# Kernel tuning notes

Measured on AMD Instinct MI355X. Metric: run time of the kernel, lower is better.

## Reference

```python
import jax, jax.numpy as jnp
import numpy as np

N_EMBD = 1024
N_HEAD = 16
B, T = 8, 1024

def setup_inputs() -> dict:
    key = jax.random.key(0)
    ks = jax.random.split(key, 5)
    s = 0.02
    return {
        'x': jax.random.normal(ks[0], (B, T, N_EMBD), dtype=jnp.float32),
        'w_attn': jax.random.normal(ks[1], (N_EMBD, 3 * N_EMBD), dtype=jnp.float32) * s,
        'b_attn': jax.random.normal(ks[2], (3 * N_EMBD,), dtype=jnp.float32) * s,
        'w_proj': jax.random.normal(ks[3], (N_EMBD, N_EMBD), dtype=jnp.float32) * s,
        'b_proj': jax.random.normal(ks[4], (N_EMBD,), dtype=jnp.float32) * s,
    }

def reference(x, w_attn, b_attn, w_proj, b_proj):
    Bb, Tt, C = x.shape
    hd = C // N_HEAD  # head dim
    qkv = x @ w_attn + b_attn                      # [B,T,3C]
    q, k, v = jnp.split(qkv, 3, axis=2)
    # [B,T,C] -> [B,H,T,hd]
    def to_heads(t):
        return t.reshape(Bb, Tt, N_HEAD, hd).transpose(0, 2, 1, 3)
    q, k, v = to_heads(q), to_heads(k), to_heads(v)
    scale = 1.0 / jnp.sqrt(jnp.asarray(hd, dtype=x.dtype))
    att = jnp.einsum('bhqd,bhkd->bhqk', q, k) * scale  # [B,H,T,T]
    causal = jnp.tril(jnp.ones((Tt, Tt), dtype=bool))  # [T,T]
    att = jnp.where(causal[None, None, :, :], att, -jnp.inf)
    att = jax.nn.softmax(att, axis=-1)
    y = jnp.einsum('bhqk,bhkd->bhqd', att, v)          # [B,H,T,hd]
    y = y.transpose(0, 2, 1, 3).reshape(Bb, Tt, C)
    y = y @ w_proj + b_proj
    return y
```

## Files before the change

kernel.cpp:

```cpp
#include <hip/hip_runtime.h>
#include <stdint.h>

#define N_EMBD 1024
#define NHEAD  16
#define HDIM   64
#define BATCH  8
#define SEQ    1024
#define MROWS  (BATCH*SEQ)

typedef __bf16 bf16x8 __attribute__((ext_vector_type(8)));
typedef float  f32x4  __attribute__((ext_vector_type(4)));

__device__ inline unsigned short f2bf(float f) {
  uint32_t u = __float_as_uint(f);
  u += 0x7FFFu + ((u >> 16) & 1u);
  return (unsigned short)(u >> 16);
}

__device__ inline f32x4 mfma_bf16(bf16x8 a, bf16x8 b, f32x4 c) {
  return __builtin_amdgcn_mfma_f32_16x16x32_bf16(a, b, c, 0, 0, 0);
}

__device__ inline void gload_lds16(const unsigned short* g, unsigned short* l) {
  __builtin_amdgcn_global_load_lds(
      (const __attribute__((address_space(1))) void*)g,
      (__attribute__((address_space(3))) void*)l,
      16, 0, 0);
}

#define DSB __builtin_amdgcn_sched_barrier(0)
#define BARRIER __builtin_amdgcn_s_barrier()
#define VMC(n) asm volatile("s_waitcnt vmcnt(" #n ")" ::: "memory")
#define LGKM0 asm volatile("s_waitcnt lgkmcnt(0)" ::: "memory"); DSB

__global__ __launch_bounds__(256) void cast_f32_bf16(
    const float* __restrict__ in, unsigned short* __restrict__ out, int n) {
  int i = (blockIdx.x * 256 + threadIdx.x) * 4;
  if (i >= n) return;
  float4 v = *(const float4*)(in + i);
  ushort4 o;
  o.x = f2bf(v.x); o.y = f2bf(v.y); o.z = f2bf(v.z); o.w = f2bf(v.w);
  *(ushort4*)(out + i) = o;
}

__global__ __launch_bounds__(256) void transpose_cast2(
    const float* __restrict__ wa, unsigned short* __restrict__ oa,
    const float* __restrict__ wp, unsigned short* __restrict__ op) {
  __shared__ unsigned short tile[64 * 72];
  const int K = 1024;
  int bx = blockIdx.x;
  const float* in; unsigned short* out; int N;
  if (bx < 48) { in = wa; out = oa; N = 3072; }
  else         { in = wp; out = op; N = 1024; bx -= 48; }
  int k0 = blockIdx.y * 64, n0 = bx * 64;
  int t = threadIdx.x;
  {
    int col = (t & 15) * 4;
#pragma unroll
    for (int it = 0; it < 4; ++it) {
      int row = (t >> 4) + it * 16;
      float4 v = *(const float4*)(in + (size_t)(k0 + row) * N + n0 + col);
      ushort4 o;
      o.x = f2bf(v.x); o.y = f2bf(v.y); o.z = f2bf(v.z); o.w = f2bf(v.w);
      *(ushort4*)&tile[row * 72 + col] = o;
    }
  }
  __syncthreads();
  {
    int kcol = (t & 7) * 8;
#pragma unroll
    for (int it = 0; it < 2; ++it) {
      int nrow = (t >> 3) + it * 32;
      alignas(16) unsigned short tmp[8];
#pragma unroll
      for (int j = 0; j < 8; ++j) tmp[j] = tile[(kcol + j) * 72 + nrow];
      *(uint4*)(out + (size_t)(n0 + nrow) * K + k0 + kcol) = *(const uint4*)tmp;
    }
  }
}

#define GEMM98_BODY(A_, Bt_)                                                    \
  __shared__ unsigned short Asl[2][8192];                                       \
  __shared__ unsigned short Bsl[2][8192];                                       \
  const int tid = threadIdx.x;                                                  \
  const int l = tid & 63, w = tid >> 6;                                         \
  const int wr = w >> 1, wc = w & 1;                                            \
  const int g = l >> 4, fr = l & 15;                                            \
  f32x4 acc[4][4];                                                              \
  _Pragma("unroll") for (int i = 0; i < 4; ++i)                                 \
    _Pragma("unroll") for (int j = 0; j < 4; ++j)                               \
      _Pragma("unroll") for (int r = 0; r < 4; ++r) acc[i][j][r] = 0.0f;        \
  const int rr = tid >> 3;                                                      \
  const int cs = ((tid & 7) * 16) ^ ((rr & 7) << 4);                            \
  const char* srcA[4]; const char* srcB[4];                                     \
  _Pragma("unroll") for (int c = 0; c < 4; ++c) {                               \
    srcA[c] = (const char*)(A_) + (size_t)(m0 + c * 32 + rr) * 2048 + cs;       \
    srcB[c] = (const char*)(Bt_) + (size_t)(n0 + c * 32 + rr) * 2048 + cs;      \
  }                                                                             \
  const int ldso = tid * 8;                                         \
  const int arow = (wr * 64 + fr) * 128;                                        \
  const int brow = (wc * 64 + fr) * 128;                                        \
  int colk[2];                                                                  \
  colk[0] = (g * 16) ^ ((fr & 7) << 4);                                         \
  colk[1] = (64 + g * 16) ^ ((fr & 7) << 4);                                    \
  _Pragma("unroll") for (int c = 0; c < 4; ++c)                                 \
    gload_lds16((const unsigned short*)(srcA[c]), &Asl[0][ldso + c * 2048]);    \
  _Pragma("unroll") for (int c = 0; c < 4; ++c)                                 \
    gload_lds16((const unsigned short*)(srcB[c]), &Bsl[0][ldso + c * 2048]);    \
  _Pragma("unroll") for (int c = 0; c < 4; ++c)                                 \
    gload_lds16((const unsigned short*)(srcA[c] + 128), &Asl[1][ldso + c * 2048]);\
  _Pragma("unroll") for (int c = 0; c < 4; ++c)                                 \
    gload_lds16((const unsigned short*)(srcB[c] + 128), &Bsl[1][ldso + c * 2048]);\
  for (int kt = 0; kt < 16; ++kt) {                                             \
    const int cur = kt & 1;                                                     \
    if (kt < 15) { VMC(8); } else { VMC(0); }                                   \
    DSB; BARRIER; DSB;                                                          \
    _Pragma("unroll") for (int ks = 0; ks < 2; ++ks) {                          \
      bf16x8 av[4], bv[4];                                                      \
      _Pragma("unroll") for (int m = 0; m < 4; ++m)                             \
        av[m] = *(const bf16x8*)((const char*)&Asl[cur][0] + arow +             \
                                 m * 16 * 128 + colk[ks]);                      \
      _Pragma("unroll") for (int n = 0; n < 4; ++n)                             \
        bv[n] = *(const bf16x8*)((const char*)&Bsl[cur][0] + brow +             \
                                 n * 16 * 128 + colk[ks]);                      \
      _Pragma("unroll") for (int n = 0; n < 4; ++n)                             \
        _Pragma("unroll") for (int m = 0; m < 4; ++m)                           \
          acc[m][n] = mfma_bf16(av[m], bv[n], acc[m][n]);                       \
    }                                                                           \
    LGKM0; BARRIER; DSB;                                                        \
    if (kt < 14) {                                                              \
      const int ko = (kt + 2) * 128;                                            \
      _Pragma("unroll") for (int c = 0; c < 4; ++c)                             \
        gload_lds16((const unsigned short*)(srcA[c] + ko),                      \
                    &Asl[cur][ldso + c * 2048]);                                \
      _Pragma("unroll") for (int c = 0; c < 4; ++c)                             \
        gload_lds16((const unsigned short*)(srcB[c] + ko),                      \
                    &Bsl[cur][ldso + c * 2048]);                                \
    }                                                                           \
  }

__global__ __launch_bounds__(256) void gemm_qkv(
    const unsigned short* __restrict__ A, const unsigned short* __restrict__ Bt,
    const float* __restrict__ bias,
    unsigned short* __restrict__ Qo, unsigned short* __restrict__ Ko,
    unsigned short* __restrict__ VTo) {
  const int bid = blockIdx.x;
  const int xcd = bid & 7;
  const int local = bid >> 3;
  const int nchunk = local >> 6;
  const int rem = local & 63;
  const int m0 = (xcd * 8 + (rem >> 3)) * 128;
  const int n0 = (nchunk * 8 + (rem & 7)) * 128;
  GEMM98_BODY(A, Bt)
#pragma unroll
  for (int i = 0; i < 4; ++i) {
    int mb = m0 + wr * 64 + i * 16 + 4 * g;
    int bidx = mb >> 10;
    int t = mb & 1023;
#pragma unroll
    for (int j = 0; j < 4; ++j) {
      int n = n0 + wc * 64 + j * 16 + fr;
      float bv2 = bias[n];
      int part = n >> 10;
      int nn2 = n & 1023;
      int h = nn2 >> 6, d = nn2 & 63;
      if (part == 2) {
        alignas(8) unsigned short pk[4];
#pragma unroll
        for (int r = 0; r < 4; ++r) pk[r] = f2bf(acc[i][j][r] + bv2);
        *(ushort4*)&VTo[((size_t)(bidx * NHEAD + h) * HDIM + d) * SEQ + t] =
            *(const ushort4*)pk;
      } else {
        unsigned short* dst = (part == 0) ? Qo : Ko;
        float scl = (part == 0) ? 0.125f : 1.0f;
        size_t base = ((size_t)(bidx * NHEAD + h) * SEQ + t) * HDIM + d;
#pragma unroll
        for (int r = 0; r < 4; ++r)
          dst[base + (size_t)r * HDIM] = f2bf((acc[i][j][r] + bv2) * scl);
      }
    }
  }
}

__global__ __launch_bounds__(256) void gemm_proj(
    const unsigned short* __restrict__ A, const unsigned short* __restrict__ Bt,
    const float* __restrict__ bias, float* __restrict__ Out) {
  const int bid = blockIdx.x;
  const int xcd = bid & 7;
  const int local = bid >> 3;
  const int m0 = (xcd * 8 + (local >> 3)) * 128;
  const int n0 = (local & 7) * 128;
  GEMM98_BODY(A, Bt)
#pragma unroll
  for (int i = 0; i < 4; ++i) {
    int mb = m0 + wr * 64 + i * 16 + 4 * g;
#pragma unroll
    for (int j = 0; j < 4; ++j) {
      int n = n0 + wc * 64 + j * 16 + fr;
      float bv2 = bias[n];
#pragma unroll
      for (int r = 0; r < 4; ++r)
        Out[(size_t)(mb + r) * N_EMBD + n] = acc[i][j][r] + bv2;
    }
  }
}

__global__ __launch_bounds__(256) void attn_kernel(
    const unsigned short* __restrict__ Q, const unsigned short* __restrict__ Kv,
    const unsigned short* __restrict__ VT, unsigned short* __restrict__ Y) {
  __shared__ unsigned short Kt[2][4096];
  __shared__ unsigned short Vt[2][4096];
  __shared__ unsigned short p_lds[4 * 32 * 72];
  __shared__ float smx[4][32];
  int tid = threadIdx.x, l = tid & 63, w = tid >> 6;
  int bid = blockIdx.x;
  int swz = (bid & 7) * 64 + (bid >> 3);
  int bh = swz >> 2;
  int pairIdx = swz & 3;
  int b = bh >> 4, h = bh & 15;
  const unsigned short* Qb = Q + (size_t)bh * SEQ * HDIM;
  const char* Kc = (const char*)(Kv + (size_t)bh * SEQ * HDIM);
  const char* Vc = (const char*)(VT + (size_t)bh * HDIM * SEQ);
  unsigned short* pw = &p_lds[w * 32 * 72];
  const int g = l >> 4;
  const int fr = l & 15;

  const int P0 = tid * 16, P1 = tid * 16 + 4096;
  const int r0 = P0 >> 7, r1 = P1 >> 7;
  const int s0 = (P0 & 127) ^ ((r0 & 7) << 4);
  const int s1 = (P1 & 127) ^ ((r1 & 7) << 4);
  const char* Kg0 = Kc + r0 * 128 + s0;
  const char* Kg1 = Kc + r1 * 128 + s1;
  const char* Vg0 = Vc + (size_t)r0 * 2048 + s0;
  const char* Vg1 = Vc + (size_t)r1 * 2048 + s1;

  const int bc = (16 * g) ^ ((l & 7) << 4);

  for (int part = 0; part < 2; ++part) {
    const int qt = (part == 0) ? pairIdx : 7 - pairIdx;
    const int q0 = qt * 128;
    const int wq = q0 + w * 32;

    bf16x8 aq[2][2];
#pragma unroll
    for (int i = 0; i < 2; ++i)
#pragma unroll
      for (int ik = 0; ik < 2; ++ik)
        aq[i][ik] = *(const bf16x8*)&Qb[(size_t)(wq + i * 16 + fr) * HDIM + ik * 32 + 8 * g];

    float mrun[2], lpart[2];
    mrun[0] = mrun[1] = 0.0f;
    lpart[0] = lpart[1] = 0.0f;
    f32x4 acc_o[2][4];
#pragma unroll
    for (int i = 0; i < 2; ++i)
#pragma unroll
      for (int jd = 0; jd < 4; ++jd)
#pragma unroll
        for (int r = 0; r < 4; ++r) acc_o[i][jd][r] = 0.0f;

    const int n_it = (q0 + 128) >> 6;

    gload_lds16((const unsigned short*)(Kg0), &Kt[0][P0 >> 1]);
    gload_lds16((const unsigned short*)(Kg1), &Kt[0][P1 >> 1]);
    gload_lds16((const unsigned short*)(Vg0), &Vt[0][P0 >> 1]);
    gload_lds16((const unsigned short*)(Vg1), &Vt[0][P1 >> 1]);

    for (int it = 0; it < n_it; ++it) {
      const int kv0 = it << 6;
      const int cur = it & 1;
      if (it + 1 < n_it) {
        const int nx = kv0 + 64;
        gload_lds16((const unsigned short*)(Kg0 + nx * 128), &Kt[cur ^ 1][P0 >> 1]);
        gload_lds16((const unsigned short*)(Kg1 + nx * 128), &Kt[cur ^ 1][P1 >> 1]);
        gload_lds16((const unsigned short*)(Vg0 + nx * 2),   &Vt[cur ^ 1][P0 >> 1]);
        gload_lds16((const unsigned short*)(Vg1 + nx * 2),   &Vt[cur ^ 1][P1 >> 1]);
        VMC(4);
      } else {
        VMC(0);
      }
      DSB; BARRIER; DSB;

      const char* Kbuf = (const char*)Kt[cur];
      const char* Vbuf = (const char*)Vt[cur];

      f32x4 s2[2][4];
#pragma unroll
      for (int i = 0; i < 2; ++i)
#pragma unroll
        for (int j = 0; j < 4; ++j)
#pragma unroll
          for (int r = 0; r < 4; ++r) s2[i][j][r] = 0.0f;

      __builtin_amdgcn_s_setprio(1);
#pragma unroll
      for (int ik = 0; ik < 2; ++ik) {
#pragma unroll
        for (int j = 0; j < 4; ++j) {
          bf16x8 bk = *(const bf16x8*)(Kbuf + (j * 16 + fr) * 128 + (bc ^ (ik << 6)));
#pragma unroll
          for (int i = 0; i < 2; ++i) s2[i][j] = mfma_bf16(bk, aq[i][ik], s2[i][j]);
        }
      }
      __builtin_amdgcn_s_setprio(0);

      bool need_mask = (kv0 + 63) > wq;
      if (need_mask) {
#pragma unroll
        for (int i = 0; i < 2; ++i) {
          int q = wq + i * 16 + fr;
#pragma unroll
          for (int j = 0; j < 4; ++j)
#pragma unroll
            for (int r = 0; r < 4; ++r) {
              int kv = kv0 + j * 16 + 4 * g + r;
              if (kv > q) s2[i][j][r] = -3.0e38f;
            }
        }
      }

      float pmloc[2];
#pragma unroll
      for (int i = 0; i < 2; ++i) {
        float m01 = fmaxf(fmaxf(s2[i][0][0], s2[i][0][1]), fmaxf(s2[i][0][2], s2[i][0][3]));
        float m11 = fmaxf(fmaxf(s2[i][1][0], s2[i][1][1]), fmaxf(s2[i][1][2], s2[i][1][3]));
        float m21 = fmaxf(fmaxf(s2[i][2][0], s2[i][2][1]), fmaxf(s2[i][2][2], s2[i][2][3]));
        float m31 = fmaxf(fmaxf(s2[i][3][0], s2[i][3][1]), fmaxf(s2[i][3][2], s2[i][3][3]));
        pmloc[i] = fmaxf(fmaxf(m01, m11), fmaxf(m21, m31));
      }
      bool ok = (pmloc[0] <= mrun[0] + 8.0f) && (pmloc[1] <= mrun[1] + 8.0f);
      if (!__all(ok)) {
#pragma unroll
        for (int i = 0; i < 2; ++i) {
          float mm = pmloc[i];
          mm = fmaxf(mm, __shfl_xor(mm, 16, 64));
          mm = fmaxf(mm, __shfl_xor(mm, 32, 64));
          float mn = fmaxf(mrun[i], mm);
          float sc = __expf(mrun[i] - mn);
          mrun[i] = mn;
          lpart[i] *= sc;
          if (g == 0) smx[w][i * 16 + fr] = sc;
        }
        asm volatile("s_waitcnt lgkmcnt(0)" ::: "memory");
#pragma unroll
        for (int i = 0; i < 2; ++i)
#pragma unroll
          for (int r = 0; r < 4; ++r) {
            float sc = smx[w][i * 16 + 4 * g + r];
#pragma unroll
            for (int jd = 0; jd < 4; ++jd) acc_o[i][jd][r] *= sc;
          }
      }

#pragma unroll
      for (int i = 0; i < 2; ++i) {
#pragma unroll
        for (int j = 0; j < 4; ++j) {
          float p0 = __expf(s2[i][j][0] - mrun[i]);
          float p1 = __expf(s2[i][j][1] - mrun[i]);
          float p2 = __expf(s2[i][j][2] - mrun[i]);
          float p3 = __expf(s2[i][j][3] - mrun[i]);
          lpart[i] += (p0 + p1) + (p2 + p3);
          uint2 pk2;
          asm("v_cvt_pk_bf16_f32 %0, %1, %2" : "=v"(pk2.x) : "v"(p0), "v"(p1));
          asm("v_cvt_pk_bf16_f32 %0, %1, %2" : "=v"(pk2.y) : "v"(p2), "v"(p3));
          *(uint2*)&pw[(i * 16 + fr) * 72 + j * 16 + 4 * g] = pk2;
        }
      }

      __builtin_amdgcn_s_setprio(1);
#pragma unroll
      for (int ik2 = 0; ik2 < 2; ++ik2) {
        bf16x8 ap[2];
#pragma unroll
        for (int i = 0; i < 2; ++i)
          ap[i] = *(const bf16x8*)&pw[(i * 16 + fr) * 72 + ik2 * 32 + 8 * g];
#pragma unroll
        for (int jd = 0; jd < 4; ++jd) {
          bf16x8 bv = *(const bf16x8*)(Vbuf + (jd * 16 + fr) * 128 + (bc ^ (ik2 << 6)));
#pragma unroll
          for (int i = 0; i < 2; ++i) acc_o[i][jd] = mfma_bf16(ap[i], bv, acc_o[i][jd]);
        }
      }
      __builtin_amdgcn_s_setprio(0);

      asm volatile("s_waitcnt lgkmcnt(0)" ::: "memory");
      DSB; BARRIER; DSB;
    }

#pragma unroll
    for (int i = 0; i < 2; ++i) {
      float t = lpart[i];
      t += __shfl_xor(t, 16, 64);
      t += __shfl_xor(t, 32, 64);
      if (g == 0) smx[w][i * 16 + fr] = t;
    }
    asm volatile("s_waitcnt lgkmcnt(0)" ::: "memory");
#pragma unroll
    for (int i = 0; i < 2; ++i)
#pragma unroll
      for (int r = 0; r < 4; ++r) {
        float inv = 1.0f / smx[w][i * 16 + 4 * g + r];
        int q = wq + i * 16 + 4 * g + r;
#pragma unroll
        for (int jd = 0; jd < 4; ++jd)
          Y[((size_t)b * SEQ + q) * N_EMBD + h * HDIM + jd * 16 + fr] =
              f2bf(acc_o[i][jd][r] * inv);
      }
  }
}

extern "C" void kernel_launch(void* const* d_in, const int* in_sizes, int n_in,
                              void* d_out, int out_size, void* d_ws, size_t ws_size,
                              hipStream_t stream) {
  (void)in_sizes; (void)n_in; (void)out_size; (void)ws_size;
  const float* x      = (const float*)d_in[0];
  const float* w_attn = (const float*)d_in[1];
  const float* b_attn = (const float*)d_in[2];
  const float* w_proj = (const float*)d_in[3];
  const float* b_proj = (const float*)d_in[4];
  float* out = (float*)d_out;

  char* ws = (char*)d_ws;
  size_t off = 0;
  auto carve = [&](size_t bytes) -> char* {
    char* p = ws + off;
    off += (bytes + 255) & ~(size_t)255;
    return p;
  };
  unsigned short* xb     = (unsigned short*)carve((size_t)MROWS * N_EMBD * 2);
  unsigned short* wTattn = (unsigned short*)carve((size_t)3 * N_EMBD * N_EMBD * 2);
  unsigned short* wTproj = (unsigned short*)carve((size_t)N_EMBD * N_EMBD * 2);
  unsigned short* Qb     = (unsigned short*)carve((size_t)MROWS * N_EMBD * 2);
  unsigned short* Kb     = (unsigned short*)carve((size_t)MROWS * N_EMBD * 2);
  unsigned short* VTb    = (unsigned short*)carve((size_t)MROWS * N_EMBD * 2);
  unsigned short* Yb     = (unsigned short*)carve((size_t)MROWS * N_EMBD * 2);
  carve(4096);

  cast_f32_bf16<<<dim3(MROWS * N_EMBD / 1024), 256, 0, stream>>>(x, xb, MROWS * N_EMBD);
  transpose_cast2<<<dim3(64, 16), 256, 0, stream>>>(w_attn, wTattn, w_proj, wTproj);
  gemm_qkv<<<dim3(1536), 256, 0, stream>>>(xb, wTattn, b_attn, Qb, Kb, VTb);
  attn_kernel<<<dim3(512), 256, 0, stream>>>(Qb, Kb, VTb, Yb);
  gemm_proj<<<dim3(512), 256, 0, stream>>>(Yb, wTproj, b_proj, out);
}
```

Before: 141.6 us.

## Merge prep kernels, enlarge QKV GEMM tile to 256x128, use exp2 softmax

Fuses the x cast and the weight transpose-cast into one prep launch, which removes a kernel launch. The QKV GEMM now uses 256x128 tiles with a single LDS buffer and a launch-bounds occupancy hint, so it runs half as many blocks, each reusing A more. It drops the double-buffered prefetch in favour of two syncthreads per k-step, which exposes load latency. Attention folds log2(e) into the Q scale and uses exp2f, with the rescale threshold adjusted to match, so the softmax exponent is cheaper.

```diff
diff --git a/kernel.cpp b/kernel.cpp
--- a/kernel.cpp
+++ b/kernel.cpp
@@ -33,27 +33,29 @@
 #define VMC(n) asm volatile("s_waitcnt vmcnt(" #n ")" ::: "memory")
 #define LGKM0 asm volatile("s_waitcnt lgkmcnt(0)" ::: "memory"); DSB
 
-__global__ __launch_bounds__(256) void cast_f32_bf16(
-    const float* __restrict__ in, unsigned short* __restrict__ out, int n) {
-  int i = (blockIdx.x * 256 + threadIdx.x) * 4;
-  if (i >= n) return;
-  float4 v = *(const float4*)(in + i);
-  ushort4 o;
-  o.x = f2bf(v.x); o.y = f2bf(v.y); o.z = f2bf(v.z); o.w = f2bf(v.w);
-  *(ushort4*)(out + i) = o;
-}
-
-__global__ __launch_bounds__(256) void transpose_cast2(
+__global__ __launch_bounds__(256) void prep_kernel(
+    const float* __restrict__ x, unsigned short* __restrict__ xb,
     const float* __restrict__ wa, unsigned short* __restrict__ oa,
     const float* __restrict__ wp, unsigned short* __restrict__ op) {
+  int bid = blockIdx.x;
+  int t = threadIdx.x;
+  if (bid < 8192) {
+    int i = (bid * 256 + t) * 4;
+    float4 v = *(const float4*)(x + i);
+    ushort4 o;
+    o.x = f2bf(v.x); o.y = f2bf(v.y); o.z = f2bf(v.z); o.w = f2bf(v.w);
+    *(ushort4*)(xb + i) = o;
+    return;
+  }
   __shared__ unsigned short tile[64 * 72];
+  int idx = bid - 8192;
+  int bx = idx & 63;
+  int ky = idx >> 6;
   const int K = 1024;
-  int bx = blockIdx.x;
   const float* in; unsigned short* out; int N;
   if (bx < 48) { in = wa; out = oa; N = 3072; }
   else         { in = wp; out = op; N = 1024; bx -= 48; }
-  int k0 = blockIdx.y * 64, n0 = bx * 64;
-  int t = threadIdx.x;
+  int k0 = ky * 64, n0 = bx * 64;
   {
     int col = (t & 15) * 4;
 #pragma unroll
@@ -79,82 +81,83 @@
   }
 }
 
-#define GEMM98_BODY(A_, Bt_)                                                    \
-  __shared__ unsigned short Asl[2][8192];                                       \
-  __shared__ unsigned short Bsl[2][8192];                                       \
-  const int tid = threadIdx.x;                                                  \
-  const int l = tid & 63, w = tid >> 6;                                         \
-  const int wr = w >> 1, wc = w & 1;                                            \
-  const int g = l >> 4, fr = l & 15;                                            \
-  f32x4 acc[4][4];                                                              \
-  _Pragma("unroll") for (int i = 0; i < 4; ++i)                                 \
-    _Pragma("unroll") for (int j = 0; j < 4; ++j)                               \
-      _Pragma("unroll") for (int r = 0; r < 4; ++r) acc[i][j][r] = 0.0f;        \
-  const int rr = tid >> 3;                                                      \
-  const int cs = ((tid & 7) * 16) ^ ((rr & 7) << 4);                            \
-  const char* srcA[4]; const char* srcB[4];                                     \
-  _Pragma("unroll") for (int c = 0; c < 4; ++c) {                               \
-    srcA[c] = (const char*)(A_) + (size_t)(m0 + c * 32 + rr) * 2048 + cs;       \
-    srcB[c] = (const char*)(Bt_) + (size_t)(n0 + c * 32 + rr) * 2048 + cs;      \
-  }                                                                             \
-  const int ldso = tid * 8;                                         \
-  const int arow = (wr * 64 + fr) * 128;                                        \
-  const int brow = (wc * 64 + fr) * 128;                                        \
-  int colk[2];                                                                  \
-  colk[0] = (g * 16) ^ ((fr & 7) << 4);                                         \
-  colk[1] = (64 + g * 16) ^ ((fr & 7) << 4);                                    \
-  _Pragma("unroll") for (int c = 0; c < 4; ++c)                                 \
-    gload_lds16((const unsigned short*)(srcA[c]), &Asl[0][ldso + c * 2048]);    \
-  _Pragma("unroll") for (int c = 0; c < 4; ++c)                                 \
-    gload_lds16((const unsigned short*)(srcB[c]), &Bsl[0][ldso + c * 2048]);    \
-  _Pragma("unroll") for (int c = 0; c < 4; ++c)                                 \
-    gload_lds16((const unsigned short*)(srcA[c] + 128), &Asl[1][ldso + c * 2048]);\
-  _Pragma("unroll") for (int c = 0; c < 4; ++c)                                 \
-    gload_lds16((const unsigned short*)(srcB[c] + 128), &Bsl[1][ldso + c * 2048]);\
-  for (int kt = 0; kt < 16; ++kt) {                                             \
-    const int cur = kt & 1;                                                     \
-    if (kt < 15) { VMC(8); } else { VMC(0); }                                   \
-    DSB; BARRIER; DSB;                                                          \
-    _Pragma("unroll") for (int ks = 0; ks < 2; ++ks) {                          \
-      bf16x8 av[4], bv[4];                                                      \
-      _Pragma("unroll") for (int m = 0; m < 4; ++m)                             \
-        av[m] = *(const bf16x8*)((const char*)&Asl[cur][0] + arow +             \
-                                 m * 16 * 128 + colk[ks]);                      \
-      _Pragma("unroll") for (int n = 0; n < 4; ++n)                             \
-        bv[n] = *(const bf16x8*)((const char*)&Bsl[cur][0] + brow +             \
-                                 n * 16 * 128 + colk[ks]);                      \
-      _Pragma("unroll") for (int n = 0; n < 4; ++n)                             \
-        _Pragma("unroll") for (int m = 0; m < 4; ++m)                           \
-          acc[m][n] = mfma_bf16(av[m], bv[n], acc[m][n]);                       \
-    }                                                                           \
-    LGKM0; BARRIER; DSB;                                                        \
-    if (kt < 14) {                                                              \
-      const int ko = (kt + 2) * 128;                                            \
-      _Pragma("unroll") for (int c = 0; c < 4; ++c)                             \
-        gload_lds16((const unsigned short*)(srcA[c] + ko),                      \
-                    &Asl[cur][ldso + c * 2048]);                                \
-      _Pragma("unroll") for (int c = 0; c < 4; ++c)                             \
-        gload_lds16((const unsigned short*)(srcB[c] + ko),                      \
-                    &Bsl[cur][ldso + c * 2048]);                                \
-    }                                                                           \
-  }
-
-__global__ __launch_bounds__(256) void gemm_qkv(
+__global__ __launch_bounds__(256, 3) void gemm_qkv(
     const unsigned short* __restrict__ A, const unsigned short* __restrict__ Bt,
     const float* __restrict__ bias,
     unsigned short* __restrict__ Qo, unsigned short* __restrict__ Ko,
     unsigned short* __restrict__ VTo) {
+  __shared__ unsigned short Asl[256 * 64];
+  __shared__ unsigned short Bsl[128 * 64];
   const int bid = blockIdx.x;
   const int xcd = bid & 7;
   const int local = bid >> 3;
-  const int nchunk = local >> 6;
-  const int rem = local & 63;
-  const int m0 = (xcd * 8 + (rem >> 3)) * 128;
+  const int nchunk = local >> 5;
+  const int rem = local & 31;
+  const int m0 = (xcd * 4 + (rem >> 3)) * 256;
   const int n0 = (nchunk * 8 + (rem & 7)) * 128;
-  GEMM98_BODY(A, Bt)
-#pragma unroll
-  for (int i = 0; i < 4; ++i) {
-    int mb = m0 + wr * 64 + i * 16 + 4 * g;
+  const int tid = threadIdx.x;
+  const int l = tid & 63, w = tid >> 6;
+  const int wr = w >> 1, wc = w & 1;
+  const int g = l >> 4, fr = l & 15;
+  f32x4 acc[8][4];
+#pragma unroll
+  for (int i = 0; i < 8; ++i)
+#pragma unroll
+    for (int j = 0; j < 4; ++j)
+#pragma unroll
+      for (int r = 0; r < 4; ++r) acc[i][j][r] = 0.0f;
+  const int rr = tid >> 3;
+  const int cs = ((tid & 7) * 16) ^ ((rr & 7) << 4);
+  const char* srcA[8];
+  const char* srcB[4];
+#pragma unroll
+  for (int c = 0; c < 8; ++c)
+    srcA[c] = (const char*)A + (size_t)(m0 + c * 32 + rr) * 2048 + cs;
+#pragma unroll
+  for (int c = 0; c < 4; ++c)
+    srcB[c] = (const char*)Bt + (size_t)(n0 + c * 32 + rr) * 2048 + cs;
+  const int ldso = tid * 8;
+  const int arow = (wr * 128 + fr) * 128;
+  const int brow = (wc * 64 + fr) * 128;
+  int colk[2];
+  colk[0] = (g * 16) ^ ((fr & 7) << 4);
+  colk[1] = (64 + g * 16) ^ ((fr & 7) << 4);
+  for (int kt = 0; kt < 16; ++kt) {
+    __syncthreads();
+#pragma unroll
+    for (int c = 0; c < 8; ++c)
+      gload_lds16((const unsigned short*)(srcA[c] + kt * 128), &Asl[ldso + c * 2048]);
+#pragma unroll
+    for (int c = 0; c < 4; ++c)
+      gload_lds16((const unsigned short*)(srcB[c] + kt * 128), &Bsl[ldso + c * 2048]);
+    __syncthreads();
+#pragma unroll
+    for (int ks = 0; ks < 2; ++ks) {
+      bf16x8 bv[4], av[4];
+#pragma unroll
+      for (int n = 0; n < 4; ++n)
+        bv[n] = *(const bf16x8*)((const char*)Bsl + brow + n * 16 * 128 + colk[ks]);
+#pragma unroll
+      for (int m = 0; m < 4; ++m)
+        av[m] = *(const bf16x8*)((const char*)Asl + arow + m * 16 * 128 + colk[ks]);
+#pragma unroll
+      for (int n = 0; n < 4; ++n)
+#pragma unroll
+        for (int m = 0; m < 4; ++m)
+          acc[m][n] = mfma_bf16(av[m], bv[n], acc[m][n]);
+#pragma unroll
+      for (int m = 0; m < 4; ++m)
+        av[m] = *(const bf16x8*)((const char*)Asl + arow + (m + 4) * 16 * 128 + colk[ks]);
+#pragma unroll
+      for (int n = 0; n < 4; ++n)
+#pragma unroll
+        for (int m = 0; m < 4; ++m)
+          acc[m + 4][n] = mfma_bf16(av[m], bv[n], acc[m + 4][n]);
+    }
+  }
+#pragma unroll
+  for (int i = 0; i < 8; ++i) {
+    int mb = m0 + wr * 128 + i * 16 + 4 * g;
     int bidx = mb >> 10;
     int t = mb & 1023;
 #pragma unroll
@@ -172,7 +175,7 @@
             *(const ushort4*)pk;
       } else {
         unsigned short* dst = (part == 0) ? Qo : Ko;
-        float scl = (part == 0) ? 0.125f : 1.0f;
+        float scl = (part == 0) ? 0.18033688f : 1.0f;
         size_t base = ((size_t)(bidx * NHEAD + h) * SEQ + t) * HDIM + d;
 #pragma unroll
         for (int r = 0; r < 4; ++r)
@@ -185,12 +188,80 @@
 __global__ __launch_bounds__(256) void gemm_proj(
     const unsigned short* __restrict__ A, const unsigned short* __restrict__ Bt,
     const float* __restrict__ bias, float* __restrict__ Out) {
+  __shared__ unsigned short Asl[2][8192];
+  __shared__ unsigned short Bsl[2][8192];
   const int bid = blockIdx.x;
   const int xcd = bid & 7;
   const int local = bid >> 3;
   const int m0 = (xcd * 8 + (local >> 3)) * 128;
   const int n0 = (local & 7) * 128;
-  GEMM98_BODY(A, Bt)
+  const int tid = threadIdx.x;
+  const int l = tid & 63, w = tid >> 6;
+  const int wr = w >> 1, wc = w & 1;
+  const int g = l >> 4, fr = l & 15;
+  f32x4 acc[4][4];
+#pragma unroll
+  for (int i = 0; i < 4; ++i)
+#pragma unroll
+    for (int j = 0; j < 4; ++j)
+#pragma unroll
+      for (int r = 0; r < 4; ++r) acc[i][j][r] = 0.0f;
+  const int rr = tid >> 3;
+  const int cs = ((tid & 7) * 16) ^ ((rr & 7) << 4);
+  const char* srcA[4]; const char* srcB[4];
+#pragma unroll
+  for (int c = 0; c < 4; ++c) {
+    srcA[c] = (const char*)A + (size_t)(m0 + c * 32 + rr) * 2048 + cs;
+    srcB[c] = (const char*)Bt + (size_t)(n0 + c * 32 + rr) * 2048 + cs;
+  }
+  const int ldso = tid * 8;
+  const int arow = (wr * 64 + fr) * 128;
+  const int brow = (wc * 64 + fr) * 128;
+  int colk[2];
+  colk[0] = (g * 16) ^ ((fr & 7) << 4);
+  colk[1] = (64 + g * 16) ^ ((fr & 7) << 4);
+#pragma unroll
+  for (int c = 0; c < 4; ++c)
+    gload_lds16((const unsigned short*)(srcA[c]), &Asl[0][ldso + c * 2048]);
+#pragma unroll
+  for (int c = 0; c < 4; ++c)
+    gload_lds16((const unsigned short*)(srcB[c]), &Bsl[0][ldso + c * 2048]);
+#pragma unroll
+  for (int c = 0; c < 4; ++c)
+    gload_lds16((const unsigned short*)(srcA[c] + 128), &Asl[1][ldso + c * 2048]);
+#pragma unroll
+  for (int c = 0; c < 4; ++c)
+    gload_lds16((const unsigned short*)(srcB[c] + 128), &Bsl[1][ldso + c * 2048]);
+  for (int kt = 0; kt < 16; ++kt) {
+    const int cur = kt & 1;
+    if (kt < 15) { VMC(8); } else { VMC(0); }
+    DSB; BARRIER; DSB;
+#pragma unroll
+    for (int ks = 0; ks < 2; ++ks) {
+      bf16x8 av[4], bv[4];
+#pragma unroll
+      for (int m = 0; m < 4; ++m)
+        av[m] = *(const bf16x8*)((const char*)&Asl[cur][0] + arow + m * 16 * 128 + colk[ks]);
+#pragma unroll
+      for (int n = 0; n < 4; ++n)
+        bv[n] = *(const bf16x8*)((const char*)&Bsl[cur][0] + brow + n * 16 * 128 + colk[ks]);
+#pragma unroll
+      for (int n = 0; n < 4; ++n)
+#pragma unroll
+        for (int m = 0; m < 4; ++m)
+          acc[m][n] = mfma_bf16(av[m], bv[n], acc[m][n]);
+    }
+    LGKM0; BARRIER; DSB;
+    if (kt < 14) {
+      const int ko = (kt + 2) * 128;
+#pragma unroll
+      for (int c = 0; c < 4; ++c)
+        gload_lds16((const unsigned short*)(srcA[c] + ko), &Asl[cur][ldso + c * 2048]);
+#pragma unroll
+      for (int c = 0; c < 4; ++c)
+        gload_lds16((const unsigned short*)(srcB[c] + ko), &Bsl[cur][ldso + c * 2048]);
+    }
+  }
 #pragma unroll
   for (int i = 0; i < 4; ++i) {
     int mb = m0 + wr * 64 + i * 16 + 4 * g;
@@ -328,7 +399,7 @@
         float m31 = fmaxf(fmaxf(s2[i][3][0], s2[i][3][1]), fmaxf(s2[i][3][2], s2[i][3][3]));
         pmloc[i] = fmaxf(fmaxf(m01, m11), fmaxf(m21, m31));
       }
-      bool ok = (pmloc[0] <= mrun[0] + 8.0f) && (pmloc[1] <= mrun[1] + 8.0f);
+      bool ok = (pmloc[0] <= mrun[0] + 11.5409f) && (pmloc[1] <= mrun[1] + 11.5409f);
       if (!__all(ok)) {
 #pragma unroll
         for (int i = 0; i < 2; ++i) {
@@ -336,7 +407,7 @@
           mm = fmaxf(mm, __shfl_xor(mm, 16, 64));
           mm = fmaxf(mm, __shfl_xor(mm, 32, 64));
           float mn = fmaxf(mrun[i], mm);
-          float sc = __expf(mrun[i] - mn);
+          float sc = exp2f(mrun[i] - mn);
           mrun[i] = mn;
           lpart[i] *= sc;
           if (g == 0) smx[w][i * 16 + fr] = sc;
@@ -356,10 +427,10 @@
       for (int i = 0; i < 2; ++i) {
 #pragma unroll
         for (int j = 0; j < 4; ++j) {
-          float p0 = __expf(s2[i][j][0] - mrun[i]);
-          float p1 = __expf(s2[i][j][1] - mrun[i]);
-          float p2 = __expf(s2[i][j][2] - mrun[i]);
-          float p3 = __expf(s2[i][j][3] - mrun[i]);
+          float p0 = exp2f(s2[i][j][0] - mrun[i]);
+          float p1 = exp2f(s2[i][j][1] - mrun[i]);
+          float p2 = exp2f(s2[i][j][2] - mrun[i]);
+          float p3 = exp2f(s2[i][j][3] - mrun[i]);
           lpart[i] += (p0 + p1) + (p2 + p3);
           uint2 pk2;
           asm("v_cvt_pk_bf16_f32 %0, %1, %2" : "=v"(pk2.x) : "v"(p0), "v"(p1));
@@ -437,9 +508,8 @@
   unsigned short* Yb     = (unsigned short*)carve((size_t)MROWS * N_EMBD * 2);
   carve(4096);
 
-  cast_f32_bf16<<<dim3(MROWS * N_EMBD / 1024), 256, 0, stream>>>(x, xb, MROWS * N_EMBD);
-  transpose_cast2<<<dim3(64, 16), 256, 0, stream>>>(w_attn, wTattn, w_proj, wTproj);
-  gemm_qkv<<<dim3(1536), 256, 0, stream>>>(xb, wTattn, b_attn, Qb, Kb, VTb);
+  prep_kernel<<<dim3(8192 + 1024), 256, 0, stream>>>(x, xb, w_attn, wTattn, w_proj, wTproj);
+  gemm_qkv<<<dim3(768), 256, 0, stream>>>(xb, wTattn, b_attn, Qb, Kb, VTb);
   attn_kernel<<<dim3(512), 256, 0, stream>>>(Qb, Kb, VTb, Yb);
   gemm_proj<<<dim3(512), 256, 0, stream>>>(Yb, wTproj, b_proj, out);
 }
```

Result: slower. 144.9 us (+2.3%).
